# Kernel tuning notes

Hardware: AMD Instinct MI355X
Metric: run time of the kernel (lower is better)

Reference implementation:

```python
import jax, jax.numpy as jnp
import numpy as np

N_NODES = 50000
N_EDGES = 800000
N_GRAPHS = 64
F_IN = 256
F_HID = 256
F_OUT = 128


def setup_inputs() -> dict:
    key = jax.random.key(0)
    ks = jax.random.split(key, 8)
    x = jax.random.normal(ks[0], (N_NODES, F_IN), jnp.float32)
    edge_index = jax.random.randint(ks[1], (2, N_EDGES), 0, N_NODES, jnp.int32)
    batch = jnp.sort(jax.random.randint(ks[2], (N_NODES,), 0, N_GRAPHS, jnp.int32))
    W1 = jax.random.normal(ks[3], (F_IN, F_HID), jnp.float32) / np.sqrt(F_IN)
    b1 = jnp.zeros((F_HID,), jnp.float32)
    W2 = jax.random.normal(ks[4], (F_HID, F_HID), jnp.float32) / np.sqrt(F_HID)
    b2 = jnp.zeros((F_HID,), jnp.float32)
    Wfc = jax.random.normal(ks[5], (3 * F_HID, F_OUT), jnp.float32) / np.sqrt(3 * F_HID)
    bfc = jnp.zeros((F_OUT,), jnp.float32)
    return {"x": x, "edge_index": edge_index, "batch": batch, "n_graphs": N_GRAPHS,
            "W1": W1, "b1": b1, "W2": W2, "b2": b2, "Wfc": Wfc, "bfc": bfc}


def _gcn_layer(h, src, dst, norm, W, b, n_nodes):
    # transform first (F_in -> F_out), then gather-normalize-scatter
    h = h @ W                                      # [N, F]
    msg = h[src] * norm[:, None]                   # [E+N, F]
    agg = jax.ops.segment_sum(msg, dst, num_segments=n_nodes)
    return agg + b


def reference(x, edge_index, batch, n_graphs, W1, b1, W2, b2, Wfc, bfc):
    n = x.shape[0]
    # eval mode: dropout_adj / F.dropout are identity
    loops = jnp.arange(n, dtype=edge_index.dtype)
    src = jnp.concatenate([edge_index[0], loops])  # A + I
    dst = jnp.concatenate([edge_index[1], loops])
    # symmetric normalization D^-1/2 (A+I) D^-1/2 (degree counted at dst)
    deg = jax.ops.segment_sum(jnp.ones_like(dst, jnp.float32), dst, num_segments=n)
    dinv = jax.lax.rsqrt(jnp.maximum(deg, 1.0))    # deg >= 1 (self loops)
    norm = dinv[src] * dinv[dst]

    h = jax.nn.relu(_gcn_layer(x, src, dst, norm, W1, b1, n))
    h = jax.nn.relu(_gcn_layer(h, src, dst, norm, W2, b2, n))

    # triple global pooling over graph ids
    sums = jax.ops.segment_sum(h, batch, num_segments=n_graphs)           # add pool
    cnts = jax.ops.segment_sum(jnp.ones((n,), h.dtype), batch, num_segments=n_graphs)
    mean = sums / jnp.maximum(cnts, 1.0)[:, None]                          # mean pool
    mx = jax.ops.segment_max(h, batch, num_segments=n_graphs)             # max pool
    mx = jnp.where(jnp.isfinite(mx), mx, 0.0)                              # empty-segment guard

    g = jnp.concatenate([mean, mx, sums], axis=1)  # [G, 3*F_HID]
    return g @ Wfc + bfc
```

## Files before the change

kernel.cpp:

```cpp
#include <hip/hip_runtime.h>

#define N_NODES 50000
#define N_EDGES 800000
#define N_GRAPHS 64
#define F 256
#define F_OUT 128
#define G_DIM 768
#define SCAN_NB ((N_NODES + 255) / 256)
#define POOL_CHUNKS 32
#define EBLK4 ((N_EDGES + 1023) / 1024)

typedef unsigned short ushort_t;
typedef short short8 __attribute__((ext_vector_type(8)));
typedef unsigned short ushort8 __attribute__((ext_vector_type(8)));
typedef unsigned short ushort4v __attribute__((ext_vector_type(4)));
typedef float float4v __attribute__((ext_vector_type(4)));
typedef float f32x2 __attribute__((ext_vector_type(2)));
typedef unsigned int uint4v __attribute__((ext_vector_type(4)));
typedef unsigned int uint2v __attribute__((ext_vector_type(2)));

__device__ __forceinline__ unsigned short f2bf(float f) {
    unsigned int u = __float_as_uint(f);
    u += 0x7FFFu + ((u >> 16) & 1u);
    return (unsigned short)(u >> 16);
}
__device__ __forceinline__ float bf2f(unsigned short s) {
    return __uint_as_float(((unsigned int)s) << 16);
}

__device__ __forceinline__ unsigned char fp8_enc(float v) {
#if __has_builtin(__builtin_amdgcn_cvt_pk_fp8_f32)
    return (unsigned char)__builtin_amdgcn_cvt_pk_fp8_f32(v, v, 0, false);
#else
    float x = v * 0x1p-120f;
    unsigned int u = __float_as_uint(x);
    unsigned int mag = u & 0x7FFFFFFFu;
    unsigned int r = mag + 0x0007FFFFu + ((mag >> 20) & 1u);
    unsigned int em = r >> 20;
    if (em > 0x7Eu) em = 0x7Eu;
    return (unsigned char)(em | ((u >> 24) & 0x80u));
#endif
}

__device__ __forceinline__ void fp8x4_dec(unsigned int u, float* o) {
#if __has_builtin(__builtin_amdgcn_cvt_pk_f32_fp8)
    f32x2 d0 = __builtin_amdgcn_cvt_pk_f32_fp8((int)u, false);
    f32x2 d1 = __builtin_amdgcn_cvt_pk_f32_fp8((int)u, true);
    o[0] = d0[0]; o[1] = d0[1]; o[2] = d1[0]; o[3] = d1[1];
#else
#pragma unroll
    for (int i = 0; i < 4; ++i) {
        unsigned int b = (u >> (8 * i)) & 0xFFu;
        unsigned int bits = ((b & 0x7Fu) << 20) | ((b & 0x80u) << 24);
        o[i] = __uint_as_float(bits) * 0x1p+120f;
    }
#endif
}

__device__ __forceinline__ void gld_lds16(const void* gsrc, void* ldst) {
    __builtin_amdgcn_global_load_lds(
        (const __attribute__((address_space(1))) unsigned int*)gsrc,
        (__attribute__((address_space(3))) unsigned int*)ldst, 16, 0, 0);
}

__global__ void prep_w_deg(const float* __restrict__ W1, const float* __restrict__ W2,
                           short* __restrict__ hi1, short* __restrict__ hi2,
                           const int* __restrict__ dst, int* __restrict__ deg,
                           int* __restrict__ rank) {
    int blk = blockIdx.x;
    if (blk < 512) {
        const float* W = (blk < 256) ? W1 : W2;
        short* hi = (blk < 256) ? hi1 : hi2;
        int n = blk & 255;
        int k = threadIdx.x;
        hi[n * 256 + k] = (short)f2bf(W[k * 256 + n]);
    } else {
        int eb = (blk - 512) * 1024 + threadIdx.x * 4;
        if (eb < N_EDGES) {
            int4 d4 = *(const int4*)&dst[eb];
            int r0 = atomicAdd(&deg[d4.x], 1);
            int r1 = atomicAdd(&deg[d4.y], 1);
            int r2 = atomicAdd(&deg[d4.z], 1);
            int r3 = atomicAdd(&deg[d4.w], 1);
            *(int4*)&rank[eb] = make_int4(r0, r1, r2, r3);
        }
    }
}

__global__ void scan_blocks(const int* __restrict__ deg, int* __restrict__ row_ptr,
                            int* __restrict__ block_tot, float* __restrict__ dinv) {
    __shared__ int sd[256];
    int t = threadIdx.x;
    int idx = blockIdx.x * 256 + t;
    int v = (idx < N_NODES) ? deg[idx] : 0;
    if (idx < N_NODES) dinv[idx] = rsqrtf((float)(v + 1));
    sd[t] = v;
    __syncthreads();
    for (int off = 1; off < 256; off <<= 1) {
        int a = (t >= off) ? sd[t - off] : 0;
        __syncthreads();
        sd[t] += a;
        __syncthreads();
    }
    if (idx < N_NODES) row_ptr[idx] = sd[t] - v;
    if (t == 255) block_tot[blockIdx.x] = sd[255];
}

__global__ void add_offsets(int* __restrict__ row_ptr, const int* __restrict__ block_tot,
                            const float* __restrict__ dinv, int2* __restrict__ rpd) {
    __shared__ int sd[256];
    int t = threadIdx.x;
    int blk = blockIdx.x;
    sd[t] = (t < blk && t < SCAN_NB) ? block_tot[t] : 0;
    __syncthreads();
    for (int off = 128; off > 0; off >>= 1) {
        if (t < off) sd[t] += sd[t + off];
        __syncthreads();
    }
    int base = sd[0];
    int idx = blk * 256 + t;
    if (idx < N_NODES) {
        int fin = row_ptr[idx] + base;
        row_ptr[idx] = fin;
        rpd[idx] = make_int2(fin, __float_as_int(dinv[idx]));
    }
    if (idx == 0) row_ptr[N_NODES] = N_EDGES;
}

#define BM 64
#define BK 32
__global__ __launch_bounds__(256) void gemm1_bucket(
        const float* __restrict__ A,
        const short* __restrict__ Bthi,
        unsigned char* __restrict__ h8, int M,
        const int* __restrict__ src, const int* __restrict__ dst,
        const float* __restrict__ dinv, const int* __restrict__ rank,
        const int2* __restrict__ rpd, unsigned int* __restrict__ erec, int ngemm) {
    __shared__ short sAh[BM * BK];
    __shared__ short sBh[256 * BK];

    if (blockIdx.x >= ngemm) {
        int eb = (blockIdx.x - ngemm) * 1024 + threadIdx.x * 4;
        if (eb < N_EDGES) {
            int4 d4 = *(const int4*)&dst[eb];
            int4 s4 = *(const int4*)&src[eb];
            int4 r4 = *(const int4*)&rank[eb];
            int dd[4] = {d4.x, d4.y, d4.z, d4.w};
            int ss[4] = {s4.x, s4.y, s4.z, s4.w};
            int rk[4] = {r4.x, r4.y, r4.z, r4.w};
            int2 rd[4];
#pragma unroll
            for (int i = 0; i < 4; ++i) rd[i] = rpd[dd[i]];
            float dv[4];
#pragma unroll
            for (int i = 0; i < 4; ++i) dv[i] = dinv[ss[i]];
#pragma unroll
            for (int i = 0; i < 4; ++i) {
                unsigned int w = (unsigned int)f2bf(__int_as_float(rd[i].y) * dv[i]);
                erec[rd[i].x + rk[i]] = (unsigned int)ss[i] | (w << 16);
            }
        }
        return;
    }

    int tid = threadIdx.x;
    int wave = tid >> 6, lane = tid & 63;
    int q = lane >> 4, t = lane & 15;
    int row0 = blockIdx.x * BM;
    int wc = wave * 64;

    int lrow = lane >> 2;
    int lk = (lane & 3) * 8;
    int ar = tid >> 2;
    int ak = (tid & 3) * 8;

    int ga = row0 + ar; if (ga >= M) ga = M - 1;
    const float* abase = &A[(size_t)ga * 256 + ak];
    float4 a0 = *(const float4*)(abase);
    float4 a1 = *(const float4*)(abase + 4);

    float4v acc[4][4] = {};
    for (int kt = 0; kt < 256; kt += BK) {
#pragma unroll
        for (int j = 0; j < 4; ++j) {
            int n = wave * 64 + j * 16 + lrow;
            size_t boff = (size_t)n * 256 + kt + lk;
            int ldso = wave * 2048 + j * 512 + lane * 8;
            gld_lds16(&Bthi[boff], &sBh[ldso]);
        }
        {
            short8 h;
            h[0] = (short)f2bf(a0.x); h[1] = (short)f2bf(a0.y);
            h[2] = (short)f2bf(a0.z); h[3] = (short)f2bf(a0.w);
            h[4] = (short)f2bf(a1.x); h[5] = (short)f2bf(a1.y);
            h[6] = (short)f2bf(a1.z); h[7] = (short)f2bf(a1.w);
            *(short8*)&sAh[ar * BK + ak] = h;
        }
        float4 na0 = a0, na1 = a1;
        if (kt + BK < 256) {
            na0 = *(const float4*)(abase + kt + BK);
            na1 = *(const float4*)(abase + kt + BK + 4);
        }
        __syncthreads();
        short8 ah[4], bh[4];
#pragma unroll
        for (int mi = 0; mi < 4; ++mi) {
            int r = mi * 16 + t;
            ah[mi] = *(const short8*)&sAh[r * BK + q * 8];
        }
#pragma unroll
        for (int ni = 0; ni < 4; ++ni) {
            int n = wc + ni * 16 + t;
            bh[ni] = *(const short8*)&sBh[n * BK + q * 8];
        }
#pragma unroll
        for (int mi = 0; mi < 4; ++mi)
#pragma unroll
            for (int ni = 0; ni < 4; ++ni)
                acc[mi][ni] = __builtin_amdgcn_mfma_f32_16x16x32_bf16(ah[mi], bh[ni], acc[mi][ni], 0, 0, 0);
        __syncthreads();
        a0 = na0; a1 = na1;
    }
#pragma unroll
    for (int mi = 0; mi < 4; ++mi) {
        int gr0 = row0 + mi * 16 + q * 4;
#pragma unroll
        for (int rr = 0; rr < 4; ++rr) {
            int gr = gr0 + rr;
            if (gr < M) {
#pragma unroll
                for (int ni = 0; ni < 4; ++ni)
                    h8[(size_t)gr * 256 + wc + ni * 16 + t] = fp8_enc(acc[mi][ni][rr]);
            }
        }
    }
}

__global__ __launch_bounds__(256) void gemm_mfma_fp8a(
        const unsigned char* __restrict__ A,
        const short* __restrict__ Bthi,
        unsigned char* __restrict__ h8, int M) {
    __shared__ short sA[BM * BK];
    __shared__ short sBh[256 * BK];
    int tid = threadIdx.x;
    int wave = tid >> 6, lane = tid & 63;
    int q = lane >> 4, t = lane & 15;
    int row0 = blockIdx.x * BM;
    int wc = wave * 64;

    int lrow = lane >> 2;
    int lk = (lane & 3) * 8;
    int ar = tid >> 2;
    int ak = (tid & 3) * 8;

    int ga = row0 + ar; if (ga >= M) ga = M - 1;
    const unsigned char* abase = &A[(size_t)ga * 256 + ak];
    uint2v areg[8];
#pragma unroll
    for (int i = 0; i < 8; ++i) areg[i] = *(const uint2v*)(abase + i * BK);

    float4v acc[4][4] = {};
#pragma unroll
    for (int ki = 0; ki < 8; ++ki) {
        int kt = ki * BK;
#pragma unroll
        for (int j = 0; j < 4; ++j) {
            int n = wave * 64 + j * 16 + lrow;
            size_t boff = (size_t)n * 256 + kt + lk;
            int ldso = wave * 2048 + j * 512 + lane * 8;
            gld_lds16(&Bthi[boff], &sBh[ldso]);
        }
        {
            float f0[4], f1[4];
            fp8x4_dec(areg[ki][0], f0);
            fp8x4_dec(areg[ki][1], f1);
            short8 h;
            h[0] = (short)f2bf(f0[0]); h[1] = (short)f2bf(f0[1]);
            h[2] = (short)f2bf(f0[2]); h[3] = (short)f2bf(f0[3]);
            h[4] = (short)f2bf(f1[0]); h[5] = (short)f2bf(f1[1]);
            h[6] = (short)f2bf(f1[2]); h[7] = (short)f2bf(f1[3]);
            *(short8*)&sA[ar * BK + ak] = h;
        }
        __syncthreads();
        short8 ah[4], bh[4];
#pragma unroll
        for (int mi = 0; mi < 4; ++mi) {
            int r = mi * 16 + t;
            ah[mi] = *(const short8*)&sA[r * BK + q * 8];
        }
#pragma unroll
        for (int ni = 0; ni < 4; ++ni) {
            int n = wc + ni * 16 + t;
            bh[ni] = *(const short8*)&sBh[n * BK + q * 8];
        }
#pragma unroll
        for (int mi = 0; mi < 4; ++mi)
#pragma unroll
            for (int ni = 0; ni < 4; ++ni)
                acc[mi][ni] = __builtin_amdgcn_mfma_f32_16x16x32_bf16(ah[mi], bh[ni], acc[mi][ni], 0, 0, 0);
        __syncthreads();
    }
#pragma unroll
    for (int mi = 0; mi < 4; ++mi) {
        int gr0 = row0 + mi * 16 + q * 4;
#pragma unroll
        for (int rr = 0; rr < 4; ++rr) {
            int gr = gr0 + rr;
            if (gr < M) {
#pragma unroll
                for (int ni = 0; ni < 4; ++ni)
                    h8[(size_t)gr * 256 + wc + ni * 16 + t] = fp8_enc(acc[mi][ni][rr]);
            }
        }
    }
}

__global__ __launch_bounds__(256) void gather_fp8(
        const int* __restrict__ row_ptr, const unsigned int* __restrict__ erec,
        const float* __restrict__ dinv,
        const unsigned char* __restrict__ h8, const float* __restrict__ b,
        unsigned char* __restrict__ out8) {
    int wave = threadIdx.x >> 6;
    int node = blockIdx.x * 4 + wave;
    int lane = threadIdx.x & 63;
    int g = lane >> 4;
    int hl = lane & 15;
    int beg = row_ptr[node], end = row_ptr[node + 1];
    float dd = dinv[node];
    float acc[16] = {};
    for (int cbeg = beg; cbeg < end; cbeg += 64) {
        int n = end - cbeg; if (n > 64) n = 64;
        unsigned int ev = 0u;
        if (lane < n) ev = __builtin_nontemporal_load(&erec[cbeg + lane]);
        int niter = (n + 15) & ~15;
        for (int k = 0; k < niter; k += 16) {
            unsigned int er0 = (unsigned int)__shfl((int)ev, k + g);
            unsigned int er1 = (unsigned int)__shfl((int)ev, k + 4 + g);
            unsigned int er2 = (unsigned int)__shfl((int)ev, k + 8 + g);
            unsigned int er3 = (unsigned int)__shfl((int)ev, k + 12 + g);
            uint4v p0 = *(const uint4v*)&h8[(size_t)((er0 & 0xFFFFu) * 256u + (unsigned)hl * 16u)];
            uint4v p1 = *(const uint4v*)&h8[(size_t)((er1 & 0xFFFFu) * 256u + (unsigned)hl * 16u)];
            uint4v p2 = *(const uint4v*)&h8[(size_t)((er2 & 0xFFFFu) * 256u + (unsigned)hl * 16u)];
            uint4v p3 = *(const uint4v*)&h8[(size_t)((er3 & 0xFFFFu) * 256u + (unsigned)hl * 16u)];
            float w0 = bf2f((unsigned short)(er0 >> 16));
            float w1 = bf2f((unsigned short)(er1 >> 16));
            float w2 = bf2f((unsigned short)(er2 >> 16));
            float w3 = bf2f((unsigned short)(er3 >> 16));
            float d0[4], d1[4], d2[4], d3[4];
#pragma unroll
            for (int wdi = 0; wdi < 4; ++wdi) {
                fp8x4_dec(p0[wdi], d0);
                fp8x4_dec(p1[wdi], d1);
                fp8x4_dec(p2[wdi], d2);
                fp8x4_dec(p3[wdi], d3);
#pragma unroll
                for (int j = 0; j < 4; ++j) {
                    int a = wdi * 4 + j;
                    acc[a] = fmaf(d0[j], w0, acc[a]);
                    acc[a] = fmaf(d1[j], w1, acc[a]);
                    acc[a] = fmaf(d2[j], w2, acc[a]);
                    acc[a] = fmaf(d3[j], w3, acc[a]);
                }
            }
        }
    }
#pragma unroll
    for (int j = 0; j < 16; ++j) {
        acc[j] += __shfl_xor(acc[j], 16);
        acc[j] += __shfl_xor(acc[j], 32);
    }
    if (g == 0) {
        uint4v sp = *(const uint4v*)&h8[(size_t)node * 256 + hl * 16];
        float sf[16];
        fp8x4_dec(sp[0], &sf[0]);
        fp8x4_dec(sp[1], &sf[4]);
        fp8x4_dec(sp[2], &sf[8]);
        fp8x4_dec(sp[3], &sf[12]);
        float4 b0 = *(const float4*)&b[hl * 16];
        float4 b1 = *(const float4*)&b[hl * 16 + 4];
        float4 b2 = *(const float4*)&b[hl * 16 + 8];
        float4 b3 = *(const float4*)&b[hl * 16 + 12];
        float bb[16] = {b0.x, b0.y, b0.z, b0.w, b1.x, b1.y, b1.z, b1.w,
                        b2.x, b2.y, b2.z, b2.w, b3.x, b3.y, b3.z, b3.w};
        float ws = dd * dd;
        uint4v o;
#pragma unroll
        for (int wd = 0; wd < 4; ++wd) {
            unsigned int packed = 0;
#pragma unroll
            for (int j = 0; j < 4; ++j) {
                int a = wd * 4 + j;
                float v = fmaxf(fmaf(sf[a], ws, acc[a]) + bb[a], 0.f);
                packed |= ((unsigned int)fp8_enc(v)) << (8 * j);
            }
            o[wd] = packed;
        }
        __builtin_nontemporal_store(o, (uint4v*)&out8[(size_t)node * 256 + hl * 16]);
    }
}

__global__ __launch_bounds__(64) void pool_partial(
        const unsigned char* __restrict__ h, const int* __restrict__ batch,
        float* __restrict__ psum, int* __restrict__ pmaxi) {
    int g = blockIdx.x;
    int chunk = blockIdx.y;
    int lane = threadIdx.x;
    int lo = 0, hi = N_NODES;
    while (lo < hi) { int mid = (lo + hi) >> 1; if (batch[mid] < g) lo = mid + 1; else hi = mid; }
    int start = lo;
    lo = 0; hi = N_NODES;
    while (lo < hi) { int mid = (lo + hi) >> 1; if (batch[mid] < g + 1) lo = mid + 1; else hi = mid; }
    int end = lo;
    int len = end - start;
    if (len <= 0) return;
    int per = (len + POOL_CHUNKS - 1) / POOL_CHUNKS;
    int cs = start + chunk * per;
    int ce = cs + per; if (ce > end) ce = end;
    if (cs >= ce) return;
    float4 sum = make_float4(0.f, 0.f, 0.f, 0.f);
    float4 mx  = make_float4(0.f, 0.f, 0.f, 0.f);
    for (int n = cs; n < ce; ++n) {
        unsigned int u = *(const unsigned int*)&h[(size_t)n * 256 + lane * 4];
        float f[4];
        fp8x4_dec(u, f);
        sum.x += f[0]; sum.y += f[1]; sum.z += f[2]; sum.w += f[3];
        mx.x = fmaxf(mx.x, f[0]); mx.y = fmaxf(mx.y, f[1]);
        mx.z = fmaxf(mx.z, f[2]); mx.w = fmaxf(mx.w, f[3]);
    }
    float* ps = &psum[g * F + lane * 4];
    atomicAdd(&ps[0], sum.x); atomicAdd(&ps[1], sum.y);
    atomicAdd(&ps[2], sum.z); atomicAdd(&ps[3], sum.w);
    int* pm = &pmaxi[g * F + lane * 4];
    atomicMax(&pm[0], __float_as_int(mx.x)); atomicMax(&pm[1], __float_as_int(mx.y));
    atomicMax(&pm[2], __float_as_int(mx.z)); atomicMax(&pm[3], __float_as_int(mx.w));
}

__global__ void final_gemm(const float* __restrict__ psum, const int* __restrict__ pmaxi,
                           const int* __restrict__ batch,
                           const float* __restrict__ Wfc, const float* __restrict__ bfc,
                           float* __restrict__ out) {
    int g = blockIdx.x;
    int o = threadIdx.x;
    __shared__ float row[G_DIM];
    __shared__ int s_cnt;
    if (threadIdx.x == 0) {
        int lo = 0, hi = N_NODES;
        while (lo < hi) { int mid = (lo + hi) >> 1; if (batch[mid] < g) lo = mid + 1; else hi = mid; }
        int start = lo;
        lo = 0; hi = N_NODES;
        while (lo < hi) { int mid = (lo + hi) >> 1; if (batch[mid] < g + 1) lo = mid + 1; else hi = mid; }
        s_cnt = lo - start;
    }
    __syncthreads();
    float inv = 1.0f / fmaxf((float)s_cnt, 1.0f);
    for (int i = threadIdx.x; i < F; i += 128) {
        float s = psum[g * F + i];
        row[i]       = s * inv;
        row[F + i]   = __int_as_float(pmaxi[g * F + i]);
        row[2*F + i] = s;
    }
    __syncthreads();
    float acc = bfc[o];
    for (int k = 0; k < G_DIM; ++k) acc += row[k] * Wfc[k * F_OUT + o];
    out[g * F_OUT + o] = acc;
}

extern "C" void kernel_launch(void* const* d_in, const int* in_sizes, int n_in,
                              void* d_out, int out_size, void* d_ws, size_t ws_size,
                              hipStream_t stream) {
    const float* x    = (const float*)d_in[0];
    const int*   ei   = (const int*)d_in[1];
    const int*   batch= (const int*)d_in[2];
    const float* W1   = (const float*)d_in[4];
    const float* b1   = (const float*)d_in[5];
    const float* W2   = (const float*)d_in[6];
    const float* b2   = (const float*)d_in[7];
    const float* Wfc  = (const float*)d_in[8];
    const float* bfc  = (const float*)d_in[9];
    float* out = (float*)d_out;

    const int* src = ei;
    const int* dst = ei + N_EDGES;

    const size_t NF = (size_t)N_NODES * F;

    unsigned char* h8   = (unsigned char*)d_ws;
    unsigned char* h1_8 = h8 + NF;
    unsigned char* h2_8 = h1_8;
    short* w1hi  = (short*)(h1_8 + NF);
    short* w2hi  = w1hi + 65536;
    float* dinv  = (float*)(w2hi + 65536);
    int*   deg   = (int*)(dinv + N_NODES);
    float* psum  = (float*)(deg + N_NODES);
    int*   pmaxi = (int*)(psum + N_GRAPHS * F);
    int2*  rpd   = (int2*)(pmaxi + N_GRAPHS * F);
    int*   row_ptr = (int*)(rpd + N_NODES);
    int*   btot  = row_ptr + N_NODES + 1;
    unsigned int* erec = (unsigned int*)(btot + 256 + 1);
    int*   rank  = (int*)(erec + N_EDGES);

    hipMemsetAsync(deg, 0, (N_NODES + 2 * N_GRAPHS * F) * sizeof(int), stream);
    prep_w_deg<<<512 + EBLK4, 256, 0, stream>>>(
        W1, W2, w1hi, w2hi, dst, deg, rank);
    scan_blocks<<<SCAN_NB, 256, 0, stream>>>(deg, row_ptr, btot, dinv);
    add_offsets<<<SCAN_NB, 256, 0, stream>>>(row_ptr, btot, dinv, rpd);

    int ggemm = (N_NODES + BM - 1) / BM;
    int ngb = N_NODES / 4;

    gemm1_bucket<<<ggemm + EBLK4, 256, 0, stream>>>(
        x, w1hi, h8, N_NODES, src, dst, dinv, rank, rpd, erec, ggemm);
    gather_fp8<<<ngb, 256, 0, stream>>>(row_ptr, erec, dinv, h8, b1, h1_8);

    gemm_mfma_fp8a<<<ggemm, 256, 0, stream>>>(h1_8, w2hi, h8, N_NODES);
    gather_fp8<<<ngb, 256, 0, stream>>>(row_ptr, erec, dinv, h8, b2, h2_8);

    pool_partial<<<dim3(N_GRAPHS, POOL_CHUNKS), 64, 0, stream>>>(h2_8, batch, psum, pmaxi);
    final_gemm<<<N_GRAPHS, F_OUT, 0, stream>>>(psum, pmaxi, batch, Wfc, bfc, out);
}
```

Baseline: 311.4 us.

## Split first GEMM across degree-count and bucketing kernels; deepen gather unroll

The first-layer GEMM is split into two halves by row. The first half runs alongside the W2 conversion and the degree-count atomics, and the second half runs alongside edge bucketing after the scan. The goal is to fill the small, latency-bound preprocessing launches with GEMM work so their cost is hidden. Separately, the gather loop now issues 8 outstanding row loads per iteration instead of 4 to raise memory-level parallelism, at the cost of more registers and more padding work when a node has few edges.

```diff
diff --git a/kernel.cpp b/kernel.cpp
--- a/kernel.cpp
+++ b/kernel.cpp
@@ -9,6 +9,9 @@
 #define SCAN_NB ((N_NODES + 255) / 256)
 #define POOL_CHUNKS 32
 #define EBLK4 ((N_EDGES + 1023) / 1024)
+#define HALF1 25024
+#define G1 (HALF1 / 64)
+#define G2 ((N_NODES - HALF1 + 63) / 64)
 
 typedef unsigned short ushort_t;
 typedef short short8 __attribute__((ext_vector_type(8)));
@@ -63,28 +66,10 @@
         (__attribute__((address_space(3))) unsigned int*)ldst, 16, 0, 0);
 }
 
-__global__ void prep_w_deg(const float* __restrict__ W1, const float* __restrict__ W2,
-                           short* __restrict__ hi1, short* __restrict__ hi2,
-                           const int* __restrict__ dst, int* __restrict__ deg,
-                           int* __restrict__ rank) {
-    int blk = blockIdx.x;
-    if (blk < 512) {
-        const float* W = (blk < 256) ? W1 : W2;
-        short* hi = (blk < 256) ? hi1 : hi2;
-        int n = blk & 255;
-        int k = threadIdx.x;
-        hi[n * 256 + k] = (short)f2bf(W[k * 256 + n]);
-    } else {
-        int eb = (blk - 512) * 1024 + threadIdx.x * 4;
-        if (eb < N_EDGES) {
-            int4 d4 = *(const int4*)&dst[eb];
-            int r0 = atomicAdd(&deg[d4.x], 1);
-            int r1 = atomicAdd(&deg[d4.y], 1);
-            int r2 = atomicAdd(&deg[d4.z], 1);
-            int r3 = atomicAdd(&deg[d4.w], 1);
-            *(int4*)&rank[eb] = make_int4(r0, r1, r2, r3);
-        }
-    }
+__global__ void prep_w1(const float* __restrict__ W1, short* __restrict__ hi1) {
+    int n = blockIdx.x;
+    int k = threadIdx.x;
+    hi1[n * 256 + k] = (short)f2bf(W1[k * 256 + n]);
 }
 
 __global__ void scan_blocks(const int* __restrict__ deg, int* __restrict__ row_ptr,
@@ -129,16 +114,122 @@
 
 #define BM 64
 #define BK 32
-__global__ __launch_bounds__(256) void gemm1_bucket(
-        const float* __restrict__ A,
-        const short* __restrict__ Bthi,
-        unsigned char* __restrict__ h8, int M,
+__device__ __forceinline__ void gemm1_body(
+        const float* __restrict__ A, const short* __restrict__ Bthi,
+        unsigned char* __restrict__ h8, int rowbase,
+        short* sAh, short* sBh) {
+    int tid = threadIdx.x;
+    int wave = tid >> 6, lane = tid & 63;
+    int q = lane >> 4, t = lane & 15;
+    int row0 = rowbase + blockIdx.x * BM;
+    int wc = wave * 64;
+
+    int lrow = lane >> 2;
+    int lk = (lane & 3) * 8;
+    int ar = tid >> 2;
+    int ak = (tid & 3) * 8;
+
+    int ga = row0 + ar; if (ga >= N_NODES) ga = N_NODES - 1;
+    const float* abase = &A[(size_t)ga * 256 + ak];
+    float4 a0 = *(const float4*)(abase);
+    float4 a1 = *(const float4*)(abase + 4);
+
+    float4v acc[4][4] = {};
+    for (int kt = 0; kt < 256; kt += BK) {
+#pragma unroll
+        for (int j = 0; j < 4; ++j) {
+            int n = wave * 64 + j * 16 + lrow;
+            size_t boff = (size_t)n * 256 + kt + lk;
+            int ldso = wave * 2048 + j * 512 + lane * 8;
+            gld_lds16(&Bthi[boff], &sBh[ldso]);
+        }
+        {
+            short8 h;
+            h[0] = (short)f2bf(a0.x); h[1] = (short)f2bf(a0.y);
+            h[2] = (short)f2bf(a0.z); h[3] = (short)f2bf(a0.w);
+            h[4] = (short)f2bf(a1.x); h[5] = (short)f2bf(a1.y);
+            h[6] = (short)f2bf(a1.z); h[7] = (short)f2bf(a1.w);
+            *(short8*)&sAh[ar * BK + ak] = h;
+        }
+        float4 na0 = a0, na1 = a1;
+        if (kt + BK < 256) {
+            na0 = *(const float4*)(abase + kt + BK);
+            na1 = *(const float4*)(abase + kt + BK + 4);
+        }
+        __syncthreads();
+        short8 ah[4], bh[4];
+#pragma unroll
+        for (int mi = 0; mi < 4; ++mi) {
+            int r = mi * 16 + t;
+            ah[mi] = *(const short8*)&sAh[r * BK + q * 8];
+        }
+#pragma unroll
+        for (int ni = 0; ni < 4; ++ni) {
+            int n = wc + ni * 16 + t;
+            bh[ni] = *(const short8*)&sBh[n * BK + q * 8];
+        }
+#pragma unroll
+        for (int mi = 0; mi < 4; ++mi)
+#pragma unroll
+            for (int ni = 0; ni < 4; ++ni)
+                acc[mi][ni] = __builtin_amdgcn_mfma_f32_16x16x32_bf16(ah[mi], bh[ni], acc[mi][ni], 0, 0, 0);
+        __syncthreads();
+        a0 = na0; a1 = na1;
+    }
+#pragma unroll
+    for (int mi = 0; mi < 4; ++mi) {
+        int gr0 = row0 + mi * 16 + q * 4;
+#pragma unroll
+        for (int rr = 0; rr < 4; ++rr) {
+            int gr = gr0 + rr;
+            if (gr < N_NODES) {
+#pragma unroll
+                for (int ni = 0; ni < 4; ++ni)
+                    h8[(size_t)gr * 256 + wc + ni * 16 + t] = fp8_enc(acc[mi][ni][rr]);
+            }
+        }
+    }
+}
+
+__global__ __launch_bounds__(256) void gemm1_deg(
+        const float* __restrict__ A, const short* __restrict__ Bthi,
+        unsigned char* __restrict__ h8,
+        const float* __restrict__ W2, short* __restrict__ hi2,
+        const int* __restrict__ dst, int* __restrict__ deg, int* __restrict__ rank,
+        int ngemm) {
+    __shared__ short sAh[BM * BK];
+    __shared__ short sBh[256 * BK];
+    if (blockIdx.x >= ngemm) {
+        int b2 = blockIdx.x - ngemm;
+        if (b2 < 256) {
+            int n = b2;
+            int k = threadIdx.x;
+            hi2[n * 256 + k] = (short)f2bf(W2[k * 256 + n]);
+        } else {
+            int eb = (b2 - 256) * 1024 + threadIdx.x * 4;
+            if (eb < N_EDGES) {
+                int4 d4 = *(const int4*)&dst[eb];
+                int r0 = atomicAdd(&deg[d4.x], 1);
+                int r1 = atomicAdd(&deg[d4.y], 1);
+                int r2 = atomicAdd(&deg[d4.z], 1);
+                int r3 = atomicAdd(&deg[d4.w], 1);
+                *(int4*)&rank[eb] = make_int4(r0, r1, r2, r3);
+            }
+        }
+        return;
+    }
+    gemm1_body(A, Bthi, h8, 0, sAh, sBh);
+}
+
+__global__ __launch_bounds__(256) void gemm1_bkt(
+        const float* __restrict__ A, const short* __restrict__ Bthi,
+        unsigned char* __restrict__ h8,
         const int* __restrict__ src, const int* __restrict__ dst,
         const float* __restrict__ dinv, const int* __restrict__ rank,
-        const int2* __restrict__ rpd, unsigned int* __restrict__ erec, int ngemm) {
+        const int2* __restrict__ rpd, unsigned int* __restrict__ erec,
+        int ngemm) {
     __shared__ short sAh[BM * BK];
     __shared__ short sBh[256 * BK];
-
     if (blockIdx.x >= ngemm) {
         int eb = (blockIdx.x - ngemm) * 1024 + threadIdx.x * 4;
         if (eb < N_EDGES) {
@@ -162,78 +253,7 @@
         }
         return;
     }
-
-    int tid = threadIdx.x;
-    int wave = tid >> 6, lane = tid & 63;
-    int q = lane >> 4, t = lane & 15;
-    int row0 = blockIdx.x * BM;
-    int wc = wave * 64;
-
-    int lrow = lane >> 2;
-    int lk = (lane & 3) * 8;
-    int ar = tid >> 2;
-    int ak = (tid & 3) * 8;
-
-    int ga = row0 + ar; if (ga >= M) ga = M - 1;
-    const float* abase = &A[(size_t)ga * 256 + ak];
-    float4 a0 = *(const float4*)(abase);
-    float4 a1 = *(const float4*)(abase + 4);
-
-    float4v acc[4][4] = {};
-    for (int kt = 0; kt < 256; kt += BK) {
-#pragma unroll
-        for (int j = 0; j < 4; ++j) {
-            int n = wave * 64 + j * 16 + lrow;
-            size_t boff = (size_t)n * 256 + kt + lk;
-            int ldso = wave * 2048 + j * 512 + lane * 8;
-            gld_lds16(&Bthi[boff], &sBh[ldso]);
-        }
-        {
-            short8 h;
-            h[0] = (short)f2bf(a0.x); h[1] = (short)f2bf(a0.y);
-            h[2] = (short)f2bf(a0.z); h[3] = (short)f2bf(a0.w);
-            h[4] = (short)f2bf(a1.x); h[5] = (short)f2bf(a1.y);
-            h[6] = (short)f2bf(a1.z); h[7] = (short)f2bf(a1.w);
-            *(short8*)&sAh[ar * BK + ak] = h;
-        }
-        float4 na0 = a0, na1 = a1;
-        if (kt + BK < 256) {
-            na0 = *(const float4*)(abase + kt + BK);
-            na1 = *(const float4*)(abase + kt + BK + 4);
-        }
-        __syncthreads();
-        short8 ah[4], bh[4];
-#pragma unroll
-        for (int mi = 0; mi < 4; ++mi) {
-            int r = mi * 16 + t;
-            ah[mi] = *(const short8*)&sAh[r * BK + q * 8];
-        }
-#pragma unroll
-        for (int ni = 0; ni < 4; ++ni) {
-            int n = wc + ni * 16 + t;
-            bh[ni] = *(const short8*)&sBh[n * BK + q * 8];
-        }
-#pragma unroll
-        for (int mi = 0; mi < 4; ++mi)
-#pragma unroll
-            for (int ni = 0; ni < 4; ++ni)
-                acc[mi][ni] = __builtin_amdgcn_mfma_f32_16x16x32_bf16(ah[mi], bh[ni], acc[mi][ni], 0, 0, 0);
-        __syncthreads();
-        a0 = na0; a1 = na1;
-    }
-#pragma unroll
-    for (int mi = 0; mi < 4; ++mi) {
-        int gr0 = row0 + mi * 16 + q * 4;
-#pragma unroll
-        for (int rr = 0; rr < 4; ++rr) {
-            int gr = gr0 + rr;
-            if (gr < M) {
-#pragma unroll
-                for (int ni = 0; ni < 4; ++ni)
-                    h8[(size_t)gr * 256 + wc + ni * 16 + t] = fp8_enc(acc[mi][ni][rr]);
-            }
-        }
-    }
+    gemm1_body(A, Bthi, h8, HALF1, sAh, sBh);
 }
 
 __global__ __launch_bounds__(256) void gemm_mfma_fp8a(
@@ -332,34 +352,28 @@
         int n = end - cbeg; if (n > 64) n = 64;
         unsigned int ev = 0u;
         if (lane < n) ev = __builtin_nontemporal_load(&erec[cbeg + lane]);
-        int niter = (n + 15) & ~15;
-        for (int k = 0; k < niter; k += 16) {
-            unsigned int er0 = (unsigned int)__shfl((int)ev, k + g);
-            unsigned int er1 = (unsigned int)__shfl((int)ev, k + 4 + g);
-            unsigned int er2 = (unsigned int)__shfl((int)ev, k + 8 + g);
-            unsigned int er3 = (unsigned int)__shfl((int)ev, k + 12 + g);
-            uint4v p0 = *(const uint4v*)&h8[(size_t)((er0 & 0xFFFFu) * 256u + (unsigned)hl * 16u)];
-            uint4v p1 = *(const uint4v*)&h8[(size_t)((er1 & 0xFFFFu) * 256u + (unsigned)hl * 16u)];
-            uint4v p2 = *(const uint4v*)&h8[(size_t)((er2 & 0xFFFFu) * 256u + (unsigned)hl * 16u)];
-            uint4v p3 = *(const uint4v*)&h8[(size_t)((er3 & 0xFFFFu) * 256u + (unsigned)hl * 16u)];
-            float w0 = bf2f((unsigned short)(er0 >> 16));
-            float w1 = bf2f((unsigned short)(er1 >> 16));
-            float w2 = bf2f((unsigned short)(er2 >> 16));
-            float w3 = bf2f((unsigned short)(er3 >> 16));
-            float d0[4], d1[4], d2[4], d3[4];
-#pragma unroll
-            for (int wdi = 0; wdi < 4; ++wdi) {
-                fp8x4_dec(p0[wdi], d0);
-                fp8x4_dec(p1[wdi], d1);
-                fp8x4_dec(p2[wdi], d2);
-                fp8x4_dec(p3[wdi], d3);
-#pragma unroll
-                for (int j = 0; j < 4; ++j) {
-                    int a = wdi * 4 + j;
-                    acc[a] = fmaf(d0[j], w0, acc[a]);
-                    acc[a] = fmaf(d1[j], w1, acc[a]);
-                    acc[a] = fmaf(d2[j], w2, acc[a]);
-                    acc[a] = fmaf(d3[j], w3, acc[a]);
+        int niter = (n + 31) & ~31;
+        for (int k = 0; k < niter; k += 32) {
+            unsigned int er[8];
+#pragma unroll
+            for (int j = 0; j < 8; ++j)
+                er[j] = (unsigned int)__shfl((int)ev, k + 4 * j + g);
+            uint4v p[8];
+#pragma unroll
+            for (int j = 0; j < 8; ++j)
+                p[j] = *(const uint4v*)&h8[(size_t)((er[j] & 0xFFFFu) * 256u + (unsigned)hl * 16u)];
+#pragma unroll
+            for (int j = 0; j < 8; ++j) {
+                float w = bf2f((unsigned short)(er[j] >> 16));
+                float d[4];
+#pragma unroll
+                for (int wdi = 0; wdi < 4; ++wdi) {
+                    fp8x4_dec(p[j][wdi], d);
+                    int a = wdi * 4;
+                    acc[a]     = fmaf(d[0], w, acc[a]);
+                    acc[a + 1] = fmaf(d[1], w, acc[a + 1]);
+                    acc[a + 2] = fmaf(d[2], w, acc[a + 2]);
+                    acc[a + 3] = fmaf(d[3], w, acc[a + 3]);
                 }
             }
         }
@@ -500,19 +514,22 @@
     int*   rank  = (int*)(erec + N_EDGES);
 
     hipMemsetAsync(deg, 0, (N_NODES + 2 * N_GRAPHS * F) * sizeof(int), stream);
-    prep_w_deg<<<512 + EBLK4, 256, 0, stream>>>(
-        W1, W2, w1hi, w2hi, dst, deg, rank);
+    prep_w1<<<256, 256, 0, stream>>>(W1, w1hi);
+
+    int ngb = N_NODES / 4;
+
+    gemm1_deg<<<G1 + 256 + EBLK4, 256, 0, stream>>>(
+        x, w1hi, h8, W2, w2hi, dst, deg, rank, G1);
+
     scan_blocks<<<SCAN_NB, 256, 0, stream>>>(deg, row_ptr, btot, dinv);
     add_offsets<<<SCAN_NB, 256, 0, stream>>>(row_ptr, btot, dinv, rpd);
 
-    int ggemm = (N_NODES + BM - 1) / BM;
-    int ngb = N_NODES / 4;
-
-    gemm1_bucket<<<ggemm + EBLK4, 256, 0, stream>>>(
-        x, w1hi, h8, N_NODES, src, dst, dinv, rank, rpd, erec, ggemm);
+    gemm1_bkt<<<G2 + EBLK4, 256, 0, stream>>>(
+        x, w1hi, h8, src, dst, dinv, rank, rpd, erec, G2);
+
     gather_fp8<<<ngb, 256, 0, stream>>>(row_ptr, erec, dinv, h8, b1, h1_8);
 
-    gemm_mfma_fp8a<<<ggemm, 256, 0, stream>>>(h1_8, w2hi, h8, N_NODES);
+    gemm_mfma_fp8a<<<(N_NODES + BM - 1) / BM, 256, 0, stream>>>(h1_8, w2hi, h8, N_NODES);
     gather_fp8<<<ngb, 256, 0, stream>>>(row_ptr, erec, dinv, h8, b2, h2_8);
 
     pool_partial<<<dim3(N_GRAPHS, POOL_CHUNKS), 64, 0, stream>>>(h2_8, batch, psum, pmaxi);
```

After: 346.9 us. 1.11x slower.
